# Performance work log

Measured on AMD Instinct MI355X. Metric: run time of the kernel, lower is better.

Reference implementation:

```python
import jax, jax.numpy as jnp
import numpy as np

MAT_MODE = ((0, 1), (0, 2), (1, 2))
VEC_MODE = (2, 1, 0)
PE_L = 6


def _sample_plane(plane, gx, gy):
    # plane: [C,H,W]; gx,gy in [-1,1]; bilinear, align_corners=True -> [C,N]
    C, H, W = plane.shape
    ix = (gx + 1.0) * 0.5 * (W - 1)
    iy = (gy + 1.0) * 0.5 * (H - 1)
    ix0 = jnp.clip(jnp.floor(ix).astype(jnp.int32), 0, W - 1)
    iy0 = jnp.clip(jnp.floor(iy).astype(jnp.int32), 0, H - 1)
    ix1 = jnp.minimum(ix0 + 1, W - 1)
    iy1 = jnp.minimum(iy0 + 1, H - 1)
    wx = ix - ix0
    wy = iy - iy0
    v00 = plane[:, iy0, ix0]
    v01 = plane[:, iy0, ix1]
    v10 = plane[:, iy1, ix0]
    v11 = plane[:, iy1, ix1]
    return (v00 * (1 - wx) * (1 - wy) + v01 * wx * (1 - wy)
            + v10 * (1 - wx) * wy + v11 * wx * wy)


def _sample_line(line, g):
    # line: [C,L]; g in [-1,1]; linear interp along L, align_corners=True -> [C,N]
    C, L = line.shape
    iy = (g + 1.0) * 0.5 * (L - 1)
    i0 = jnp.clip(jnp.floor(iy).astype(jnp.int32), 0, L - 1)
    i1 = jnp.minimum(i0 + 1, L - 1)
    w = iy - i0
    return line[:, i0] * (1 - w) + line[:, i1] * w


def _forward(points_3D, ray_unit, density_planes, density_lines,
             color_planes, color_lines, basis_W, W1, b1, W2, b2, W3, b3):
    xyz = jax.lax.stop_gradient(points_3D)  # coords are detached in original
    N = xyz.shape[0]
    # density: sum over 3 axes of (plane_feat * line_feat) summed over comps
    sigma = jnp.zeros((N,), dtype=points_3D.dtype)
    for i in range(3):
        p = _sample_plane(density_planes[i], xyz[:, MAT_MODE[i][0]], xyz[:, MAT_MODE[i][1]])
        l = _sample_line(density_lines[i], xyz[:, VEC_MODE[i]])
        sigma = sigma + jnp.sum(p * l, axis=0)
    # color feature: concat 3x16 comps -> [48,N], multiply, project to 27
    pc = jnp.concatenate([_sample_plane(color_planes[i], xyz[:, MAT_MODE[i][0]], xyz[:, MAT_MODE[i][1]]) for i in range(3)], axis=0)
    lc = jnp.concatenate([_sample_line(color_lines[i], xyz[:, VEC_MODE[i]]) for i in range(3)], axis=0)
    color_feat = (pc * lc).T @ basis_W.T  # [N,27]
    # positional encoding of view dirs, L=6
    freqs = (2.0 ** jnp.arange(PE_L, dtype=points_3D.dtype)) * np.float32(np.pi)
    spec = ray_unit[:, :, None] * freqs  # [N,3,6]
    enc = jnp.stack([jnp.sin(spec), jnp.cos(spec)], axis=-2).reshape(N, -1)  # [N,36]
    feat = jnp.concatenate([color_feat, ray_unit, enc], axis=-1)  # [N,66]
    h = jax.nn.relu(feat @ W1.T + b1)
    h = jax.nn.relu(h @ W2.T + b2)
    rgb = jax.nn.sigmoid(h @ W3.T + b3)
    return rgb, sigma


def setup_inputs():
    key = jax.random.key(0)
    ks = jax.random.split(key, 16)
    N = 1048576
    R = 128   # grid resolution per axis
    C = 16    # components per axis
    CF = 27   # color feature dim
    scale = 0.1
    points_3D = jax.random.uniform(ks[0], (N, 3), dtype=jnp.float32, minval=-1.0, maxval=1.0)
    ray = jax.random.normal(ks[1], (N, 3), dtype=jnp.float32)
    ray_unit = ray / jnp.linalg.norm(ray, axis=-1, keepdims=True)
    density_planes = scale * jax.random.normal(ks[2], (3, C, R, R), dtype=jnp.float32)
    density_lines = scale * jax.random.normal(ks[3], (3, C, R), dtype=jnp.float32)
    color_planes = scale * jax.random.normal(ks[4], (3, C, R, R), dtype=jnp.float32)
    color_lines = scale * jax.random.normal(ks[5], (3, C, R), dtype=jnp.float32)
    basis_W = jax.random.normal(ks[6], (CF, 3 * C), dtype=jnp.float32) * (1.0 / np.sqrt(3 * C))
    in_mlp = 3 + 2 * PE_L * 3 + CF  # 66
    W1 = jax.random.normal(ks[7], (128, in_mlp), dtype=jnp.float32) * (1.0 / np.sqrt(in_mlp))
    b1 = jnp.zeros((128,), dtype=jnp.float32)
    W2 = jax.random.normal(ks[8], (128, 128), dtype=jnp.float32) * (1.0 / np.sqrt(128))
    b2 = jnp.zeros((128,), dtype=jnp.float32)
    W3 = jax.random.normal(ks[9], (3, 128), dtype=jnp.float32) * (1.0 / np.sqrt(128))
    b3 = jnp.zeros((3,), dtype=jnp.float32)
    return {"points_3D": points_3D, "ray_unit": ray_unit,
            "density_planes": density_planes, "density_lines": density_lines,
            "color_planes": color_planes, "color_lines": color_lines,
            "basis_W": basis_W, "W1": W1, "b1": b1, "W2": W2, "b2": b2,
            "W3": W3, "b3": b3}


def reference(points_3D, ray_unit, density_planes, density_lines,
              color_planes, color_lines, basis_W, W1, b1, W2, b2, W3, b3):
    return _forward(points_3D, ray_unit, density_planes, density_lines,
                    color_planes, color_lines, basis_W, W1, b1, W2, b2, W3, b3)
```

## Files before the change

kernel.cpp:

```cpp
#include <hip/hip_runtime.h>

typedef _Float16 f16;
typedef f16 f16x8 __attribute__((ext_vector_type(8)));
typedef f16 f16x2 __attribute__((ext_vector_type(2)));
typedef float f32x4 __attribute__((ext_vector_type(4)));

#define PI_F 3.14159265358979323846f

constexpr int TP = 128;
constexpr int FSTR = 136;
constexpr int PLANE_ELEMS = 128 * 128 * 16;
constexpr int IPLANE = 128 * 128 * 32;
constexpr int ILINE = 128 * 32;

__global__ void prep_small(const float* __restrict__ W1, const float* __restrict__ basisW,
                           const float* __restrict__ W2, const float* __restrict__ W3,
                           const float* __restrict__ dlines, const float* __restrict__ clines,
                           f16* __restrict__ W1p, f16* __restrict__ W2h, f16* __restrict__ W3p,
                           f16* __restrict__ linesI) {
    int t = blockIdx.x * 256 + threadIdx.x;
    if (t < 128 * 96) {
        int r = t / 96, c = t % 96;
        float v = 0.f;
        if (c < 48) {
            for (int m = 0; m < 27; m++) v += W1[r * 66 + m] * basisW[m * 48 + c];
        } else if (c < 51) {
            v = W1[r * 66 + 27 + (c - 48)];
        } else if (c < 87) {
            v = W1[r * 66 + 30 + (c - 51)];
        }
        W1p[t] = (f16)v;
        return;
    }
    t -= 128 * 96;
    if (t < 128 * 128) { W2h[t] = (f16)W2[t]; return; }
    t -= 128 * 128;
    if (t < 16 * 128) {
        int r = t / 128, k = t % 128;
        W3p[t] = (f16)(r < 3 ? W3[r * 128 + k] : 0.f);
        return;
    }
    t -= 16 * 128;
    if (t < 3 * ILINE) {
        int axis = t / ILINE;
        int rem = t % ILINE;
        int l = rem / 32, c = rem % 32;
        float v = (c < 16) ? dlines[axis * 2048 + c * 128 + l]
                           : clines[axis * 2048 + (c - 16) * 128 + l];
        linesI[t] = (f16)v;
    }
}

__global__ void interleave_planes(const float* __restrict__ dplanes,
                                  const float* __restrict__ cplanes,
                                  f16* __restrict__ planesI) {
    __shared__ f16 s[128 * 34];
    int b = blockIdx.x;
    int axis = b >> 7;
    int y = b & 127;
    const float* dsrc = dplanes + (size_t)axis * PLANE_ELEMS + y * 128;
    const float* csrc = cplanes + (size_t)axis * PLANE_ELEMS + y * 128;
    int tid = threadIdx.x;
#pragma unroll
    for (int it = 0; it < 8; it++) {
        int c = it * 2 + (tid >> 7);
        int x = tid & 127;
        s[x * 34 + c]      = (f16)dsrc[(size_t)c * 16384 + x];
        s[x * 34 + 16 + c] = (f16)csrc[(size_t)c * 16384 + x];
    }
    __syncthreads();
    f16* dst = planesI + (size_t)(axis * 128 + y) * (128 * 32);
#pragma unroll
    for (int it = 0; it < 8; it++) {
        int d = it * 256 + tid;
        int x = d >> 4, cp = (d & 15) * 2;
        dst[2 * d]     = s[x * 34 + cp];
        dst[2 * d + 1] = s[x * 34 + cp + 1];
    }
}

__global__ __launch_bounds__(256, 4) void nerf_main(
    const float* __restrict__ pts, const float* __restrict__ rayu,
    const f16* __restrict__ planesI, const f16* __restrict__ linesI,
    const f16* __restrict__ W1p, const f16* __restrict__ W2h, const f16* __restrict__ W3p,
    const float* __restrict__ b1, const float* __restrict__ b2, const float* __restrict__ b3,
    float* __restrict__ out, int N) {
    __shared__ __align__(16) f16 tile[TP * FSTR];
    const int tid = threadIdx.x;
    const int p0 = blockIdx.x * TP;

    {
        const int grp = tid >> 2;
        const int q = tid & 3;
        const int qc = q - 2;
#pragma unroll
        for (int it = 0; it < 2; it++) {
            const int pi = it * 64 + grp;
            const int pp = p0 + pi;
            float g0 = pts[3 * pp + 0], g1 = pts[3 * pp + 1], g2 = pts[3 * pp + 2];
            float g[3] = {g0, g1, g2};
            float sigma = 0.f;
            f16* frow = &tile[pi * FSTR];
#pragma unroll
            for (int i = 0; i < 3; i++) {
                const int m0 = (i == 2) ? 1 : 0;
                const int m1 = (i == 0) ? 1 : 2;
                const int vm = 2 - i;
                float fx = (g[m0] + 1.f) * 0.5f * 127.f;
                float fy = (g[m1] + 1.f) * 0.5f * 127.f;
                float fl = (g[vm] + 1.f) * 0.5f * 127.f;
                int ix0 = min(max((int)floorf(fx), 0), 127); int ix1 = min(ix0 + 1, 127);
                int iy0 = min(max((int)floorf(fy), 0), 127); int iy1 = min(iy0 + 1, 127);
                int il0 = min(max((int)floorf(fl), 0), 127); int il1 = min(il0 + 1, 127);
                float wx = fx - (float)ix0, wy = fy - (float)iy0, wl = fl - (float)il0;
                f16 w00 = (f16)((1.f - wx) * (1.f - wy));
                f16 w01 = (f16)(wx * (1.f - wy));
                f16 w10 = (f16)((1.f - wx) * wy);
                f16 w11 = (f16)(wx * wy);
                f16 wl1 = (f16)(1.f - wl), wlh = (f16)wl;
                const f16* c00 = planesI + ((i * 128 + iy0) * 128 + ix0) * 32 + 8 * q;
                const f16* c01 = planesI + ((i * 128 + iy0) * 128 + ix1) * 32 + 8 * q;
                const f16* c10 = planesI + ((i * 128 + iy1) * 128 + ix0) * 32 + 8 * q;
                const f16* c11 = planesI + ((i * 128 + iy1) * 128 + ix1) * 32 + 8 * q;
                const f16* l0 = linesI + (i * 128 + il0) * 32 + 8 * q;
                const f16* l1 = linesI + (i * 128 + il1) * 32 + 8 * q;
                f16x8 v00 = *(const f16x8*)c00;
                f16x8 v01 = *(const f16x8*)c01;
                f16x8 v10 = *(const f16x8*)c10;
                f16x8 v11 = *(const f16x8*)c11;
                f16x8 pb = v00 * w00 + v01 * w01 + v10 * w10 + v11 * w11;
                f16x8 lv = *(const f16x8*)l0 * wl1 + *(const f16x8*)l1 * wlh;
                f16x8 prod = pb * lv;
                if (q < 2) {
                    const f16x2 one2 = {(f16)1.f, (f16)1.f};
#pragma unroll
                    for (int e = 0; e < 4; e++) {
                        f16x2 pr2 = {prod[2 * e], prod[2 * e + 1]};
                        sigma = __builtin_amdgcn_fdot2(pr2, one2, sigma, false);
                    }
                } else {
                    *(f16x8*)(frow + 16 * i + 8 * qc) = prod;
                }
            }
            sigma += __shfl_xor(sigma, 1);
            if (q == 0) out[3 * N + pp] = sigma;
        }
    }

    if (tid < TP) {
        const int pp = p0 + tid;
        float rx = rayu[3 * pp + 0], ry = rayu[3 * pp + 1], rz = rayu[3 * pp + 2];
        float rv[3] = {rx, ry, rz};
        f16 tail[48];
        tail[0] = (f16)rx; tail[1] = (f16)ry; tail[2] = (f16)rz;
#pragma unroll
        for (int d = 0; d < 3; d++) {
            float f = rv[d] * PI_F;
            float s = __sinf(f), c = __cosf(f);
#pragma unroll
            for (int k = 0; k < 6; k++) {
                tail[3 + 12 * d + k] = (f16)s;
                tail[3 + 12 * d + 6 + k] = (f16)c;
                float ns = 2.f * s * c;
                float nc = 1.f - 2.f * s * s;
                s = ns; c = nc;
            }
        }
#pragma unroll
        for (int e = 39; e < 48; e++) tail[e] = (f16)0.f;
#pragma unroll
        for (int j = 0; j < 6; j++)
            *(f16x8*)&tile[tid * FSTR + 48 + 8 * j] = *(const f16x8*)&tail[8 * j];
    }
    __syncthreads();

    const int w = tid >> 6, l = tid & 63, ar = l & 15, kg = l >> 4;
    const int col0 = 32 * w + ar;
    const int col1 = 32 * w + 16 + ar;

    f32x4 acc[8][2];

    {
        f16x8 bfr0[3], bfr1[3];
#pragma unroll
        for (int k = 0; k < 3; k++) {
            bfr0[k] = *(const f16x8*)(W1p + col0 * 96 + 32 * k + 8 * kg);
            bfr1[k] = *(const f16x8*)(W1p + col1 * 96 + 32 * k + 8 * kg);
        }
        float bias0 = b1[col0], bias1 = b1[col1];
#pragma unroll
        for (int m = 0; m < 8; m++) {
            acc[m][0] = (f32x4){bias0, bias0, bias0, bias0};
            acc[m][1] = (f32x4){bias1, bias1, bias1, bias1};
        }
#pragma unroll
        for (int m = 0; m < 8; m++) {
            const f16* arow = &tile[(16 * m + ar) * FSTR + 8 * kg];
#pragma unroll
            for (int k = 0; k < 3; k++) {
                f16x8 a = *(const f16x8*)(arow + 32 * k);
                acc[m][0] = __builtin_amdgcn_mfma_f32_16x16x32_f16(a, bfr0[k], acc[m][0], 0, 0, 0);
                acc[m][1] = __builtin_amdgcn_mfma_f32_16x16x32_f16(a, bfr1[k], acc[m][1], 0, 0, 0);
            }
        }
    }
    __syncthreads();
#pragma unroll
    for (int m = 0; m < 8; m++)
#pragma unroll
        for (int j = 0; j < 4; j++) {
            int row = 16 * m + 4 * kg + j;
            tile[row * FSTR + col0] = (f16)fmaxf(acc[m][0][j], 0.f);
            tile[row * FSTR + col1] = (f16)fmaxf(acc[m][1][j], 0.f);
        }
    __syncthreads();

    {
        f16x8 bfr0[4], bfr1[4];
#pragma unroll
        for (int k = 0; k < 4; k++) {
            bfr0[k] = *(const f16x8*)(W2h + col0 * 128 + 32 * k + 8 * kg);
            bfr1[k] = *(const f16x8*)(W2h + col1 * 128 + 32 * k + 8 * kg);
        }
        float bias0 = b2[col0], bias1 = b2[col1];
#pragma unroll
        for (int m = 0; m < 8; m++) {
            acc[m][0] = (f32x4){bias0, bias0, bias0, bias0};
            acc[m][1] = (f32x4){bias1, bias1, bias1, bias1};
        }
#pragma unroll
        for (int m = 0; m < 8; m++) {
            const f16* arow = &tile[(16 * m + ar) * FSTR + 8 * kg];
#pragma unroll
            for (int k = 0; k < 4; k++) {
                f16x8 a = *(const f16x8*)(arow + 32 * k);
                acc[m][0] = __builtin_amdgcn_mfma_f32_16x16x32_f16(a, bfr0[k], acc[m][0], 0, 0, 0);
                acc[m][1] = __builtin_amdgcn_mfma_f32_16x16x32_f16(a, bfr1[k], acc[m][1], 0, 0, 0);
            }
        }
    }
    __syncthreads();
#pragma unroll
    for (int m = 0; m < 8; m++)
#pragma unroll
        for (int j = 0; j < 4; j++) {
            int row = 16 * m + 4 * kg + j;
            tile[row * FSTR + col0] = (f16)fmaxf(acc[m][0][j], 0.f);
            tile[row * FSTR + col1] = (f16)fmaxf(acc[m][1][j], 0.f);
        }
    __syncthreads();

    {
        f16x8 bfr[4];
#pragma unroll
        for (int k = 0; k < 4; k++)
            bfr[k] = *(const f16x8*)(W3p + ar * 128 + 32 * k + 8 * kg);
        float bias3 = (ar < 3) ? b3[ar] : 0.f;
#pragma unroll
        for (int mm = 0; mm < 2; mm++) {
            int m = 2 * w + mm;
            f32x4 a3 = (f32x4){bias3, bias3, bias3, bias3};
#pragma unroll
            for (int k = 0; k < 4; k++) {
                f16x8 a = *(const f16x8*)&tile[(16 * m + ar) * FSTR + 32 * k + 8 * kg];
                a3 = __builtin_amdgcn_mfma_f32_16x16x32_f16(a, bfr[k], a3, 0, 0, 0);
            }
            if (ar < 3) {
#pragma unroll
                for (int j = 0; j < 4; j++) {
                    int row = p0 + 16 * m + 4 * kg + j;
                    out[3 * row + ar] = 1.f / (1.f + __expf(-a3[j]));
                }
            }
        }
    }
}

extern "C" void kernel_launch(void* const* d_in, const int* in_sizes, int n_in,
                              void* d_out, int out_size, void* d_ws, size_t ws_size,
                              hipStream_t stream) {
    const float* pts    = (const float*)d_in[0];
    const float* rayu   = (const float*)d_in[1];
    const float* dplanes = (const float*)d_in[2];
    const float* dlines  = (const float*)d_in[3];
    const float* cplanes = (const float*)d_in[4];
    const float* clines  = (const float*)d_in[5];
    const float* basisW  = (const float*)d_in[6];
    const float* W1 = (const float*)d_in[7];
    const float* b1 = (const float*)d_in[8];
    const float* W2 = (const float*)d_in[9];
    const float* b2 = (const float*)d_in[10];
    const float* W3 = (const float*)d_in[11];
    const float* b3 = (const float*)d_in[12];
    float* out = (float*)d_out;
    const int N = in_sizes[0] / 3;

    f16* planesI = (f16*)d_ws;
    f16* linesI = planesI + 3 * IPLANE;
    f16* W1p = linesI + 3 * ILINE;
    f16* W2h = W1p + 128 * 96;
    f16* W3p = W2h + 128 * 128;

    prep_small<<<168, 256, 0, stream>>>(W1, basisW, W2, W3, dlines, clines,
                                        W1p, W2h, W3p, linesI);
    interleave_planes<<<384, 256, 0, stream>>>(dplanes, cplanes, planesI);
    nerf_main<<<N / TP, 256, 0, stream>>>(pts, rayu, planesI, linesI,
                                          W1p, W2h, W3p, b1, b2, b3, out, N);
}
```

Measured before the change: 141.8 us.

## Pack MLP activations as f16 pairs with permuted weight columns, simplify sampling indices

```diff
diff --git a/kernel.cpp b/kernel.cpp
--- a/kernel.cpp
+++ b/kernel.cpp
@@ -3,6 +3,7 @@
 typedef _Float16 f16;
 typedef f16 f16x8 __attribute__((ext_vector_type(8)));
 typedef f16 f16x2 __attribute__((ext_vector_type(2)));
+typedef __fp16 h16x2 __attribute__((ext_vector_type(2)));
 typedef float f32x4 __attribute__((ext_vector_type(4)));
 
 #define PI_F 3.14159265358979323846f
@@ -12,6 +13,7 @@
 constexpr int PLANE_ELEMS = 128 * 128 * 16;
 constexpr int IPLANE = 128 * 128 * 32;
 constexpr int ILINE = 128 * 32;
+
 
 __global__ void prep_small(const float* __restrict__ W1, const float* __restrict__ basisW,
                            const float* __restrict__ W2, const float* __restrict__ W3,
@@ -33,10 +35,16 @@
         return;
     }
     t -= 128 * 96;
-    if (t < 128 * 128) { W2h[t] = (f16)W2[t]; return; }
+    if (t < 128 * 128) {
+        int n = t / 128, s = t % 128;
+        int k = (s & ~31) + ((s & 31) >> 1) + 16 * (s & 1);
+        W2h[t] = (f16)W2[n * 128 + k];
+        return;
+    }
     t -= 128 * 128;
     if (t < 16 * 128) {
-        int r = t / 128, k = t % 128;
+        int r = t / 128, s = t % 128;
+        int k = (s & ~31) + ((s & 31) >> 1) + 16 * (s & 1);
         W3p[t] = (f16)(r < 3 ? W3[r * 128 + k] : 0.f);
         return;
     }
@@ -93,6 +101,8 @@
         const int grp = tid >> 2;
         const int q = tid & 3;
         const int qc = q - 2;
+        const f16* pq = planesI + 8 * q;
+        const f16* lq = linesI + 8 * q;
 #pragma unroll
         for (int it = 0; it < 2; it++) {
             const int pi = it * 64 + grp;
@@ -106,30 +116,27 @@
                 const int m0 = (i == 2) ? 1 : 0;
                 const int m1 = (i == 0) ? 1 : 2;
                 const int vm = 2 - i;
-                float fx = (g[m0] + 1.f) * 0.5f * 127.f;
-                float fy = (g[m1] + 1.f) * 0.5f * 127.f;
-                float fl = (g[vm] + 1.f) * 0.5f * 127.f;
-                int ix0 = min(max((int)floorf(fx), 0), 127); int ix1 = min(ix0 + 1, 127);
-                int iy0 = min(max((int)floorf(fy), 0), 127); int iy1 = min(iy0 + 1, 127);
-                int il0 = min(max((int)floorf(fl), 0), 127); int il1 = min(il0 + 1, 127);
+                float fx = (g[m0] + 1.f) * 63.5f;
+                float fy = (g[m1] + 1.f) * 63.5f;
+                float fl = (g[vm] + 1.f) * 63.5f;
+                int ix0 = min((int)fx, 126);
+                int iy0 = min((int)fy, 126);
+                int il0 = min((int)fl, 126);
                 float wx = fx - (float)ix0, wy = fy - (float)iy0, wl = fl - (float)il0;
                 f16 w00 = (f16)((1.f - wx) * (1.f - wy));
                 f16 w01 = (f16)(wx * (1.f - wy));
                 f16 w10 = (f16)((1.f - wx) * wy);
                 f16 w11 = (f16)(wx * wy);
                 f16 wl1 = (f16)(1.f - wl), wlh = (f16)wl;
-                const f16* c00 = planesI + ((i * 128 + iy0) * 128 + ix0) * 32 + 8 * q;
-                const f16* c01 = planesI + ((i * 128 + iy0) * 128 + ix1) * 32 + 8 * q;
-                const f16* c10 = planesI + ((i * 128 + iy1) * 128 + ix0) * 32 + 8 * q;
-                const f16* c11 = planesI + ((i * 128 + iy1) * 128 + ix1) * 32 + 8 * q;
-                const f16* l0 = linesI + (i * 128 + il0) * 32 + 8 * q;
-                const f16* l1 = linesI + (i * 128 + il1) * 32 + 8 * q;
+                const f16* c00 = pq + ((i * 128 + iy0) * 128 + ix0) * 32;
+                const f16* c10 = c00 + 128 * 32;
+                const f16* l0 = lq + (i * 128 + il0) * 32;
                 f16x8 v00 = *(const f16x8*)c00;
-                f16x8 v01 = *(const f16x8*)c01;
+                f16x8 v01 = *(const f16x8*)(c00 + 32);
                 f16x8 v10 = *(const f16x8*)c10;
-                f16x8 v11 = *(const f16x8*)c11;
+                f16x8 v11 = *(const f16x8*)(c10 + 32);
                 f16x8 pb = v00 * w00 + v01 * w01 + v10 * w10 + v11 * w11;
-                f16x8 lv = *(const f16x8*)l0 * wl1 + *(const f16x8*)l1 * wlh;
+                f16x8 lv = *(const f16x8*)l0 * wl1 + *(const f16x8*)(l0 + 32) * wlh;
                 f16x8 prod = pb * lv;
                 if (q < 2) {
                     const f16x2 one2 = {(f16)1.f, (f16)1.f};
@@ -177,6 +184,7 @@
     const int w = tid >> 6, l = tid & 63, ar = l & 15, kg = l >> 4;
     const int col0 = 32 * w + ar;
     const int col1 = 32 * w + 16 + ar;
+    const int wbo = 32 * w + 2 * ar;
 
     f32x4 acc[8][2];
 
@@ -210,8 +218,9 @@
 #pragma unroll
         for (int j = 0; j < 4; j++) {
             int row = 16 * m + 4 * kg + j;
-            tile[row * FSTR + col0] = (f16)fmaxf(acc[m][0][j], 0.f);
-            tile[row * FSTR + col1] = (f16)fmaxf(acc[m][1][j], 0.f);
+            h16x2 pr = __builtin_amdgcn_cvt_pkrtz(fmaxf(acc[m][0][j], 0.f),
+                                                  fmaxf(acc[m][1][j], 0.f));
+            *(h16x2*)&tile[row * FSTR + wbo] = pr;
         }
     __syncthreads();
 
@@ -245,8 +254,9 @@
 #pragma unroll
         for (int j = 0; j < 4; j++) {
             int row = 16 * m + 4 * kg + j;
-            tile[row * FSTR + col0] = (f16)fmaxf(acc[m][0][j], 0.f);
-            tile[row * FSTR + col1] = (f16)fmaxf(acc[m][1][j], 0.f);
+            h16x2 pr = __builtin_amdgcn_cvt_pkrtz(fmaxf(acc[m][0][j], 0.f),
+                                                  fmaxf(acc[m][1][j], 0.f));
+            *(h16x2*)&tile[row * FSTR + wbo] = pr;
         }
     __syncthreads();
 
```

Result: faster. 136.6 us (-3.6%).
